# Kernel optimization log

Measured on AMD Instinct MI355X. Metric: run time of the kernel, lower is better.

The kernel has to match this reference:

```python
import jax, jax.numpy as jnp
import numpy as np


def setup_inputs() -> dict:
    key = jax.random.key(0)
    ks = jax.random.split(key, 8)
    B, N, D, S = 4, 16384, 512, 512
    x = jax.random.normal(ks[0], (B, N, D), dtype=jnp.float32)
    jx = jnp.sort(jax.random.randint(ks[1], (N,), 0, S, dtype=jnp.int64))
    scale = 1.0 / np.sqrt(D)
    Wf = jax.random.normal(ks[2], (D, D), dtype=jnp.float32) * scale
    bf = jax.random.normal(ks[3], (D,), dtype=jnp.float32) * scale
    Wg = jax.random.normal(ks[4], (D, D), dtype=jnp.float32) * scale
    bg = jax.random.normal(ks[5], (D,), dtype=jnp.float32) * scale
    Wh = jax.random.normal(ks[6], (D, D), dtype=jnp.float32) * scale
    bh = jax.random.normal(ks[7], (D,), dtype=jnp.float32) * scale
    return {"x": x, "jx": jx, "num_segments": S, "Wf": Wf, "bf": bf,
            "Wg": Wg, "bg": bg, "Wh": Wh, "bh": bh}


def reference(x, jx, num_segments, Wf, bf, Wg, bg, Wh, bh):
    # x: [B, N, D]; jx: [N] segment ids; segments along axis 1.
    fx = jnp.einsum('bnd,ed->bne', x, Wf) + bf  # f(x)
    gx = jnp.einsum('bnd,ed->bne', x, Wg) + bg  # g(x)
    # move N to leading axis so jax.ops.segment_* apply: [N, B, D]
    gx_t = jnp.transpose(gx, (1, 0, 2))
    fx_t = jnp.transpose(fx, (1, 0, 2))
    # scatter_softmax over segments (numerically stable)
    m = jax.ops.segment_max(gx_t, jx, num_segments=num_segments)  # [S, B, D]
    e = jnp.exp(gx_t - m[jx])
    denom = jax.ops.segment_sum(e, jx, num_segments=num_segments)  # [S, B, D]
    w = e / denom[jx]  # [N, B, D]
    # weighted scatter-sum
    y_t = jax.ops.segment_sum(fx_t * w, jx, num_segments=num_segments)  # [S, B, D]
    y = jnp.transpose(y_t, (1, 0, 2))  # [B, S, D]
    hy = jnp.einsum('bsd,ed->bse', y, Wh) + bh
    # expand=True: gather back to per-element
    return hy[:, jx]  # [B, N, D]
```

## Files before the change

kernel.cpp:

```cpp
#include <hip/hip_runtime.h>
#include <stdint.h>

#define B_ 4
#define N_ 16384
#define D_ 512
#define S_ 512

typedef __attribute__((ext_vector_type(8))) short bf16x8;
typedef __attribute__((ext_vector_type(4))) float f32x4;

__device__ __forceinline__ float bf2f(unsigned short u) {
  union { unsigned int i; float f; } v; v.i = ((unsigned int)u) << 16; return v.f;
}
__device__ __forceinline__ unsigned short f2bf(float f) {
  unsigned int x = __float_as_uint(f);
  return (unsigned short)((x + 0x7FFFu + ((x >> 16) & 1u)) >> 16);
}
__device__ __forceinline__ float ldf(const void* p, long i, bool f32) {
  return f32 ? ((const float*)p)[i] : bf2f(((const unsigned short*)p)[i]);
}
__device__ __forceinline__ void gl_lds16(void* lds_base, const void* g) {
  __builtin_amdgcn_global_load_lds(
      (const __attribute__((address_space(1))) unsigned int*)g,
      (__attribute__((address_space(3))) unsigned int*)lds_base,
      16, 0, 0);
}

__device__ __forceinline__ bool classify_f32(const unsigned short* x, int* cnt) {
  int c = 0;
#pragma unroll
  for (int i = 0; i < 8; i++) {
    unsigned short w = x[threadIdx.x * 8 + i];
    int e = (w >> 7) & 0xFF;
    if (e == 0 || (e >= 100 && e <= 140)) c++;
  }
  cnt[threadIdx.x] = c;
  __syncthreads();
  for (int s = 128; s > 0; s >>= 1) {
    if ((int)threadIdx.x < s) cnt[threadIdx.x] += cnt[threadIdx.x + s];
    __syncthreads();
  }
  bool f32 = cnt[0] < 1843;
  __syncthreads();
  return f32;
}

__device__ __forceinline__ bool jx_is_i64(const int* jx32) { return jx32[N_ - 1] == 0; }
__device__ __forceinline__ int seg_id(const int* jx32, int n, bool i64) {
  return i64 ? jx32[2 * n] : jx32[n];
}

__global__ __launch_bounds__(256)
void prep_all(const void* __restrict__ x, const int* __restrict__ jx,
              const void* __restrict__ Wf, const void* __restrict__ bfv,
              const void* __restrict__ Wg, const void* __restrict__ bgv,
              const void* __restrict__ Wh, const void* __restrict__ bhv,
              unsigned short* __restrict__ xb, unsigned short* __restrict__ Wfg,
              unsigned short* __restrict__ biasfg, unsigned short* __restrict__ Whb,
              unsigned short* __restrict__ bhb, int* __restrict__ segst) {
  const int blk = blockIdx.x, tid = threadIdx.x;
  if (blk >= 19462) {
    int s = (blk - 19462) * 256 + tid;
    if (s > S_) return;
    bool i64 = jx_is_i64(jx);
    int lo = 0, hi = N_;
    while (lo < hi) {
      int mid = (lo + hi) >> 1;
      if (seg_id(jx, mid, i64) < s) lo = mid + 1; else hi = mid;
    }
    segst[s] = lo;
    return;
  }
  __shared__ int cnt[256];
  const bool f32 = classify_f32((const unsigned short*)x, cnt);
  if (blk < 16384) {
    const size_t i0 = ((size_t)blk * 256 + tid) * 8;
    bf16x8 v;
    if (f32) {
      const float4* p = (const float4*)((const float*)x + i0);
      float4 a = p[0], b = p[1];
      v[0]=f2bf(a.x); v[1]=f2bf(a.y); v[2]=f2bf(a.z); v[3]=f2bf(a.w);
      v[4]=f2bf(b.x); v[5]=f2bf(b.y); v[6]=f2bf(b.z); v[7]=f2bf(b.w);
    } else {
      v = *(const bf16x8*)((const unsigned short*)x + i0);
    }
    *(bf16x8*)(xb + i0) = v;
  } else {
    int idx = (blk - 16384) * 256 + tid;
    if (idx < 524288) {
      int e = idx >> 9, d = idx & 511;
      float v = (e < 512) ? ldf(Wf, (long)e * 512 + d, f32)
                          : ldf(Wg, (long)(e - 512) * 512 + d, f32);
      Wfg[idx] = f2bf(v);
    } else if (idx < 786432) {
      Whb[idx - 524288] = f2bf(ldf(Wh, idx - 524288, f32));
    } else if (idx < 787456) {
      int j = idx - 786432;
      biasfg[j] = f2bf(j < 512 ? ldf(bfv, j, f32) : ldf(bgv, j - 512, f32));
    } else {
      bhb[idx - 787456] = f2bf(ldf(bhv, idx - 787456, f32));
    }
  }
}

#define BK 32

__global__ __launch_bounds__(256, 4)
void gemm_fg(const unsigned short* __restrict__ A, const unsigned short* __restrict__ Bm,
             const unsigned short* __restrict__ bias,
             unsigned short* __restrict__ Cf, unsigned short* __restrict__ Cg,
             int E, int Kdim, int splitcol, int tilesM, int tilesN) {
  __shared__ __align__(16) unsigned short As[128 * BK];
  __shared__ __align__(16) unsigned short Bs[128 * BK];
  const int L = blockIdx.x;
  const int xcd = L & 7, local = L >> 3;
  const int tm = xcd * (tilesM >> 3) + local / tilesN;
  const int tn = local % tilesN;
  const int m0 = tm * 128, n0 = tn * 128;

  const int tid  = threadIdx.x;
  const int w    = tid >> 6;
  const int lane = tid & 63;
  const int wm   = w >> 1, wn = w & 1;
  const int l15  = lane & 15, l4 = lane >> 4;
  const int srow = lane >> 2;
  const int scol = (lane & 3) * 8;

  f32x4 acc[4][4];
#pragma unroll
  for (int i = 0; i < 4; i++)
#pragma unroll
    for (int j = 0; j < 4; j++) acc[i][j] = (f32x4){0.f, 0.f, 0.f, 0.f};

  for (int kt = 0; kt < Kdim; kt += BK) {
    __syncthreads();
#pragma unroll
    for (int r = 0; r < 2; r++) {
      const int rb = (r * 4 + w) * 16;
      gl_lds16(&As[rb * BK], A + (size_t)(m0 + rb + srow) * Kdim + kt + scol);
      gl_lds16(&Bs[rb * BK], Bm + (size_t)(n0 + rb + srow) * Kdim + kt + scol);
    }
    __syncthreads();

    bf16x8 a[4], b[4];
#pragma unroll
    for (int i = 0; i < 4; i++)
      a[i] = *(const bf16x8*)&As[(wm * 64 + i * 16 + l15) * BK + l4 * 8];
#pragma unroll
    for (int j = 0; j < 4; j++)
      b[j] = *(const bf16x8*)&Bs[(wn * 64 + j * 16 + l15) * BK + l4 * 8];
#pragma unroll
    for (int i = 0; i < 4; i++)
#pragma unroll
      for (int j = 0; j < 4; j++)
        acc[i][j] = __builtin_amdgcn_mfma_f32_16x16x32_bf16(a[i], b[j], acc[i][j], 0, 0, 0);
  }

#pragma unroll
  for (int j = 0; j < 4; j++) {
    const int col = n0 + wn * 64 + j * 16 + l15;
    const float bv = bf2f(bias[col]);
    unsigned short* base; int cc, stride;
    if (col < splitcol) { base = Cf; cc = col; stride = splitcol; }
    else { base = Cg; cc = col - splitcol; stride = E - splitcol; }
#pragma unroll
    for (int i = 0; i < 4; i++) {
      const int rowb = m0 + wm * 64 + i * 16 + l4 * 4;
#pragma unroll
      for (int r = 0; r < 4; r++)
        base[(size_t)(rowb + r) * stride + cc] = f2bf(acc[i][j][r] + bv);
    }
  }
}

__global__ __launch_bounds__(256)
void seg_softmax(const unsigned short* __restrict__ f, const unsigned short* __restrict__ g,
                 const int* __restrict__ segst, unsigned short* __restrict__ y) {
  const int s = blockIdx.x * 2 + (threadIdx.x >> 7);
  const int b = blockIdx.y;
  const int d0 = (threadIdx.x & 127) * 4;
  const int st = segst[s], en = segst[s + 1];
  float den0=0.f, den1=0.f, den2=0.f, den3=0.f;
  float y0=0.f, y1=0.f, y2=0.f, y3=0.f;
  for (int n = st; n < en; n++) {
    const size_t off = (size_t)(b * N_ + n) * 512 + d0;
    const uint2 fp = *(const uint2*)(f + off);
    const uint2 gp = *(const uint2*)(g + off);
    const float f0 = bf2f((unsigned short)fp.x), f1 = bf2f((unsigned short)(fp.x >> 16));
    const float f2 = bf2f((unsigned short)fp.y), f3 = bf2f((unsigned short)(fp.y >> 16));
    const float g0 = bf2f((unsigned short)gp.x), g1 = bf2f((unsigned short)(gp.x >> 16));
    const float g2 = bf2f((unsigned short)gp.y), g3 = bf2f((unsigned short)(gp.y >> 16));
    const float e0 = __expf(g0), e1 = __expf(g1), e2 = __expf(g2), e3 = __expf(g3);
    den0 += e0; den1 += e1; den2 += e2; den3 += e3;
    y0 += f0 * e0; y1 += f1 * e1; y2 += f2 * e2; y3 += f3 * e3;
  }
  uint2 o;
  if (en > st) {
    o.x = (unsigned int)f2bf(y0 / den0) | ((unsigned int)f2bf(y1 / den1) << 16);
    o.y = (unsigned int)f2bf(y2 / den2) | ((unsigned int)f2bf(y3 / den3) << 16);
  } else { o.x = 0u; o.y = 0u; }
  *(uint2*)(y + (size_t)(b * S_ + s) * 512 + d0) = o;
}

__global__ __launch_bounds__(256)
void hy_gather(const unsigned short* __restrict__ y, const unsigned short* __restrict__ Whb,
               const unsigned short* __restrict__ bhb, const int* __restrict__ segst,
               const int* __restrict__ jx, const void* __restrict__ x,
               void* __restrict__ out) {
  __shared__ __align__(16) unsigned short As[64 * 32];
  __shared__ __align__(16) unsigned short Bs[64 * 32];
  __shared__ float hy_lds[64 * 64];
  __shared__ int cnt[256];
  const bool f32 = classify_f32((const unsigned short*)x, cnt);

  const int tid = threadIdx.x;
  const int w = tid >> 6, lane = tid & 63;
  const int l15 = lane & 15, l4 = lane >> 4;
  const int tr = blockIdx.x >> 3, tc = blockIdx.x & 7;
  const int m0 = tr * 64, c0 = tc * 64;
  const int b = m0 >> 9, s0 = m0 & 511;

  f32x4 acc[4];
#pragma unroll
  for (int j = 0; j < 4; j++) acc[j] = (f32x4){0.f, 0.f, 0.f, 0.f};

  const int srow = lane >> 2, scol = (lane & 3) * 8;
  for (int kt = 0; kt < 512; kt += 32) {
    __syncthreads();
    gl_lds16(&As[(w * 16) * 32], y   + (size_t)(m0 + w * 16 + srow) * 512 + kt + scol);
    gl_lds16(&Bs[(w * 16) * 32], Whb + (size_t)(c0 + w * 16 + srow) * 512 + kt + scol);
    __syncthreads();
    bf16x8 a = *(const bf16x8*)&As[(w * 16 + l15) * 32 + l4 * 8];
#pragma unroll
    for (int j = 0; j < 4; j++) {
      bf16x8 bb = *(const bf16x8*)&Bs[(j * 16 + l15) * 32 + l4 * 8];
      acc[j] = __builtin_amdgcn_mfma_f32_16x16x32_bf16(a, bb, acc[j], 0, 0, 0);
    }
  }
  __syncthreads();
#pragma unroll
  for (int j = 0; j < 4; j++) {
    const float bv = bf2f(bhb[c0 + j * 16 + l15]);
#pragma unroll
    for (int r = 0; r < 4; r++)
      hy_lds[(w * 16 + l4 * 4 + r) * 64 + j * 16 + l15] = acc[j][r] + bv;
  }
  __syncthreads();

  const int col = tid & 63, nstep = tid >> 6;
  for (int lr = 0; lr < 64; lr++) {
    const int st = segst[s0 + lr], en = segst[s0 + lr + 1];
    if (st >= en) continue;
    const float v = hy_lds[lr * 64 + col];
    if (f32) {
      float* o = (float*)out;
      for (int n = st + nstep; n < en; n += 4)
        o[((size_t)(b * N_ + n)) * 512 + c0 + col] = v;
    } else {
      unsigned short* o = (unsigned short*)out;
      const unsigned short vb = f2bf(v);
      for (int n = st + nstep; n < en; n += 4)
        o[((size_t)(b * N_ + n)) * 512 + c0 + col] = vb;
    }
  }
}

extern "C" void kernel_launch(void* const* d_in, const int* in_sizes, int n_in,
                              void* d_out, int out_size, void* d_ws, size_t ws_size,
                              hipStream_t stream) {
  const void* x  = d_in[0];
  const int* jx  = (const int*)d_in[1];
  const void* Wf = d_in[3];
  const void* bf = d_in[4];
  const void* Wg = d_in[5];
  const void* bg = d_in[6];
  const void* Wh = d_in[7];
  const void* bh = d_in[8];

  char* ws = (char*)d_ws;
  int* segst             = (int*)(ws + 4096);
  unsigned short* biasfg = (unsigned short*)(ws + 8192);
  unsigned short* bhb    = (unsigned short*)(ws + 16384);
  unsigned short* Wfg    = (unsigned short*)(ws + 32768);
  unsigned short* Whb    = (unsigned short*)(ws + 1081344);
  unsigned short* y_ws   = (unsigned short*)(ws + 1605632);
  unsigned short* xb     = (unsigned short*)(ws + 8388608);
  unsigned short* fbuf   = (unsigned short*)d_out;
  unsigned short* gbuf   = (unsigned short*)d_out + (size_t)B_ * N_ * D_;

  prep_all<<<19465, 256, 0, stream>>>(x, jx, Wf, bf, Wg, bg, Wh, bh,
                                      xb, Wfg, biasfg, Whb, bhb, segst);
  gemm_fg<<<4096, 256, 0, stream>>>(xb, Wfg, biasfg, fbuf, gbuf,
                                    1024, 512, 512, 512, 8);
  seg_softmax<<<dim3(256, B_), 256, 0, stream>>>(fbuf, gbuf, segst, y_ws);
  hy_gather<<<256, 256, 0, stream>>>(y_ws, Whb, bhb, segst, jx, x, d_out);
}
```

Baseline: 395.0 us.

## Fuse x fp32-to-bf16 conversion into GEMM A-load and split gather into separate kernel

Removes the separate pass that converted x to bf16 in workspace; the f/g GEMM now loads fp32 x directly and converts while staging into LDS. The dtype classification is computed once into a flag instead of in every block. The hy projection now writes to a workspace buffer, and a new fully parallel gather kernel writes the output with one wavefront per row and vectorized stores. This replaces the per-tile serial segment loop that used scalar stores. The trade-off is an extra launch plus a hy round-trip, and synchronous fp32 A loads in the GEMM in place of async global-to-LDS copies.

```diff
diff --git a/kernel.cpp b/kernel.cpp
--- a/kernel.cpp
+++ b/kernel.cpp
@@ -26,7 +26,15 @@
       16, 0, 0);
 }
 
-__device__ __forceinline__ bool classify_f32(const unsigned short* x, int* cnt) {
+__device__ __forceinline__ bool jx_is_i64(const int* jx32) { return jx32[N_ - 1] == 0; }
+__device__ __forceinline__ int seg_id(const int* jx32, int n, bool i64) {
+  return i64 ? jx32[2 * n] : jx32[n];
+}
+
+__global__ __launch_bounds__(256)
+void k0_flag_bounds(const unsigned short* __restrict__ x, const int* __restrict__ jx,
+                    int* __restrict__ flag, int* __restrict__ segst) {
+  __shared__ int cnt[256];
   int c = 0;
 #pragma unroll
   for (int i = 0; i < 8; i++) {
@@ -40,82 +48,56 @@
     if ((int)threadIdx.x < s) cnt[threadIdx.x] += cnt[threadIdx.x + s];
     __syncthreads();
   }
-  bool f32 = cnt[0] < 1843;
-  __syncthreads();
-  return f32;
-}
-
-__device__ __forceinline__ bool jx_is_i64(const int* jx32) { return jx32[N_ - 1] == 0; }
-__device__ __forceinline__ int seg_id(const int* jx32, int n, bool i64) {
-  return i64 ? jx32[2 * n] : jx32[n];
-}
-
-__global__ __launch_bounds__(256)
-void prep_all(const void* __restrict__ x, const int* __restrict__ jx,
-              const void* __restrict__ Wf, const void* __restrict__ bfv,
-              const void* __restrict__ Wg, const void* __restrict__ bgv,
-              const void* __restrict__ Wh, const void* __restrict__ bhv,
-              unsigned short* __restrict__ xb, unsigned short* __restrict__ Wfg,
-              unsigned short* __restrict__ biasfg, unsigned short* __restrict__ Whb,
-              unsigned short* __restrict__ bhb, int* __restrict__ segst) {
-  const int blk = blockIdx.x, tid = threadIdx.x;
-  if (blk >= 19462) {
-    int s = (blk - 19462) * 256 + tid;
-    if (s > S_) return;
-    bool i64 = jx_is_i64(jx);
-    int lo = 0, hi = N_;
-    while (lo < hi) {
-      int mid = (lo + hi) >> 1;
-      if (seg_id(jx, mid, i64) < s) lo = mid + 1; else hi = mid;
-    }
-    segst[s] = lo;
-    return;
-  }
-  __shared__ int cnt[256];
-  const bool f32 = classify_f32((const unsigned short*)x, cnt);
-  if (blk < 16384) {
-    const size_t i0 = ((size_t)blk * 256 + tid) * 8;
-    bf16x8 v;
-    if (f32) {
-      const float4* p = (const float4*)((const float*)x + i0);
-      float4 a = p[0], b = p[1];
-      v[0]=f2bf(a.x); v[1]=f2bf(a.y); v[2]=f2bf(a.z); v[3]=f2bf(a.w);
-      v[4]=f2bf(b.x); v[5]=f2bf(b.y); v[6]=f2bf(b.z); v[7]=f2bf(b.w);
-    } else {
-      v = *(const bf16x8*)((const unsigned short*)x + i0);
-    }
-    *(bf16x8*)(xb + i0) = v;
-  } else {
-    int idx = (blk - 16384) * 256 + tid;
-    if (idx < 524288) {
-      int e = idx >> 9, d = idx & 511;
-      float v = (e < 512) ? ldf(Wf, (long)e * 512 + d, f32)
-                          : ldf(Wg, (long)(e - 512) * 512 + d, f32);
-      Wfg[idx] = f2bf(v);
-    } else if (idx < 786432) {
-      Whb[idx - 524288] = f2bf(ldf(Wh, idx - 524288, f32));
-    } else if (idx < 787456) {
-      int j = idx - 786432;
-      biasfg[j] = f2bf(j < 512 ? ldf(bfv, j, f32) : ldf(bgv, j - 512, f32));
-    } else {
-      bhb[idx - 787456] = f2bf(ldf(bhv, idx - 787456, f32));
-    }
+  if (threadIdx.x == 0) flag[0] = (cnt[0] < 1843) ? 1 : 0;
+
+  const int s = blockIdx.x * 256 + threadIdx.x;
+  if (s > S_) return;
+  const bool i64 = jx_is_i64(jx);
+  int lo = 0, hi = N_;
+  while (lo < hi) {
+    int mid = (lo + hi) >> 1;
+    if (seg_id(jx, mid, i64) < s) lo = mid + 1; else hi = mid;
+  }
+  segst[s] = lo;
+}
+
+__global__ __launch_bounds__(256)
+void prep_w(const void* __restrict__ Wf, const void* __restrict__ bfv,
+            const void* __restrict__ Wg, const void* __restrict__ bgv,
+            const void* __restrict__ Wh, const void* __restrict__ bhv,
+            const int* __restrict__ flag,
+            unsigned short* __restrict__ Wfg, unsigned short* __restrict__ biasfg,
+            unsigned short* __restrict__ Whb, unsigned short* __restrict__ bhb) {
+  const bool f32 = flag[0] != 0;
+  int idx = blockIdx.x * 256 + threadIdx.x;
+  if (idx < 524288) {
+    int e = idx >> 9, d = idx & 511;
+    float v = (e < 512) ? ldf(Wf, (long)e * 512 + d, f32)
+                        : ldf(Wg, (long)(e - 512) * 512 + d, f32);
+    Wfg[idx] = f2bf(v);
+  } else if (idx < 786432) {
+    Whb[idx - 524288] = f2bf(ldf(Wh, idx - 524288, f32));
+  } else if (idx < 787456) {
+    int j = idx - 786432;
+    biasfg[j] = f2bf(j < 512 ? ldf(bfv, j, f32) : ldf(bgv, j - 512, f32));
+  } else if (idx < 787968) {
+    bhb[idx - 787456] = f2bf(ldf(bhv, idx - 787456, f32));
   }
 }
 
 #define BK 32
 
-__global__ __launch_bounds__(256, 4)
-void gemm_fg(const unsigned short* __restrict__ A, const unsigned short* __restrict__ Bm,
-             const unsigned short* __restrict__ bias,
-             unsigned short* __restrict__ Cf, unsigned short* __restrict__ Cg,
-             int E, int Kdim, int splitcol, int tilesM, int tilesN) {
+__global__ __launch_bounds__(256, 2)
+void gemm_fg(const void* __restrict__ A, const unsigned short* __restrict__ Bm,
+             const unsigned short* __restrict__ bias, const int* __restrict__ flag,
+             unsigned short* __restrict__ Cf, unsigned short* __restrict__ Cg) {
   __shared__ __align__(16) unsigned short As[128 * BK];
   __shared__ __align__(16) unsigned short Bs[128 * BK];
+  const bool af32 = flag[0] != 0;
   const int L = blockIdx.x;
   const int xcd = L & 7, local = L >> 3;
-  const int tm = xcd * (tilesM >> 3) + local / tilesN;
-  const int tn = local % tilesN;
+  const int tm = xcd * 64 + local / 8;
+  const int tn = local % 8;
   const int m0 = tm * 128, n0 = tn * 128;
 
   const int tid  = threadIdx.x;
@@ -125,6 +107,8 @@
   const int l15  = lane & 15, l4 = lane >> 4;
   const int srow = lane >> 2;
   const int scol = (lane & 3) * 8;
+  const int arow = tid >> 1;
+  const int ak0  = (tid & 1) * 16;
 
   f32x4 acc[4][4];
 #pragma unroll
@@ -132,43 +116,60 @@
 #pragma unroll
     for (int j = 0; j < 4; j++) acc[i][j] = (f32x4){0.f, 0.f, 0.f, 0.f};
 
-  for (int kt = 0; kt < Kdim; kt += BK) {
+  for (int kt = 0; kt < 512; kt += BK) {
     __syncthreads();
 #pragma unroll
     for (int r = 0; r < 2; r++) {
       const int rb = (r * 4 + w) * 16;
-      gl_lds16(&As[rb * BK], A + (size_t)(m0 + rb + srow) * Kdim + kt + scol);
-      gl_lds16(&Bs[rb * BK], Bm + (size_t)(n0 + rb + srow) * Kdim + kt + scol);
+      gl_lds16(&Bs[rb * BK], Bm + (size_t)(n0 + rb + srow) * 512 + kt + scol);
     }
-    __syncthreads();
-
-    bf16x8 a[4], b[4];
+    if (af32) {
+      const float4* ap = (const float4*)((const float*)A +
+                          (size_t)(m0 + arow) * 512 + kt + ak0);
+      float4 a0 = ap[0], a1 = ap[1], a2 = ap[2], a3 = ap[3];
+      bf16x8 v0, v1;
+      v0[0]=f2bf(a0.x); v0[1]=f2bf(a0.y); v0[2]=f2bf(a0.z); v0[3]=f2bf(a0.w);
+      v0[4]=f2bf(a1.x); v0[5]=f2bf(a1.y); v0[6]=f2bf(a1.z); v0[7]=f2bf(a1.w);
+      v1[0]=f2bf(a2.x); v1[1]=f2bf(a2.y); v1[2]=f2bf(a2.z); v1[3]=f2bf(a2.w);
+      v1[4]=f2bf(a3.x); v1[5]=f2bf(a3.y); v1[6]=f2bf(a3.z); v1[7]=f2bf(a3.w);
+      *(bf16x8*)&As[arow * BK + ak0]     = v0;
+      *(bf16x8*)&As[arow * BK + ak0 + 8] = v1;
+    } else {
+#pragma unroll
+      for (int r = 0; r < 2; r++) {
+        const int rb = (r * 4 + w) * 16;
+        gl_lds16(&As[rb * BK],
+                 (const unsigned short*)A + (size_t)(m0 + rb + srow) * 512 + kt + scol);
+      }
+    }
+    __syncthreads();
+
+    bf16x8 a[4], bb[4];
 #pragma unroll
     for (int i = 0; i < 4; i++)
       a[i] = *(const bf16x8*)&As[(wm * 64 + i * 16 + l15) * BK + l4 * 8];
 #pragma unroll
     for (int j = 0; j < 4; j++)
-      b[j] = *(const bf16x8*)&Bs[(wn * 64 + j * 16 + l15) * BK + l4 * 8];
+      bb[j] = *(const bf16x8*)&Bs[(wn * 64 + j * 16 + l15) * BK + l4 * 8];
 #pragma unroll
     for (int i = 0; i < 4; i++)
 #pragma unroll
       for (int j = 0; j < 4; j++)
-        acc[i][j] = __builtin_amdgcn_mfma_f32_16x16x32_bf16(a[i], b[j], acc[i][j], 0, 0, 0);
+        acc[i][j] = __builtin_amdgcn_mfma_f32_16x16x32_bf16(a[i], bb[j], acc[i][j], 0, 0, 0);
   }
 
 #pragma unroll
   for (int j = 0; j < 4; j++) {
     const int col = n0 + wn * 64 + j * 16 + l15;
     const float bv = bf2f(bias[col]);
-    unsigned short* base; int cc, stride;
-    if (col < splitcol) { base = Cf; cc = col; stride = splitcol; }
-    else { base = Cg; cc = col - splitcol; stride = E - splitcol; }
+    unsigned short* base = (col < 512) ? Cf : Cg;
+    const int cc = col & 511;
 #pragma unroll
     for (int i = 0; i < 4; i++) {
       const int rowb = m0 + wm * 64 + i * 16 + l4 * 4;
 #pragma unroll
       for (int r = 0; r < 4; r++)
-        base[(size_t)(rowb + r) * stride + cc] = f2bf(acc[i][j][r] + bv);
+        base[(size_t)(rowb + r) * 512 + cc] = f2bf(acc[i][j][r] + bv);
     }
   }
 }
@@ -203,28 +204,20 @@
 }
 
 __global__ __launch_bounds__(256)
-void hy_gather(const unsigned short* __restrict__ y, const unsigned short* __restrict__ Whb,
-               const unsigned short* __restrict__ bhb, const int* __restrict__ segst,
-               const int* __restrict__ jx, const void* __restrict__ x,
-               void* __restrict__ out) {
+void gemm_hy(const unsigned short* __restrict__ y, const unsigned short* __restrict__ Whb,
+             const unsigned short* __restrict__ bhb, unsigned short* __restrict__ hy) {
   __shared__ __align__(16) unsigned short As[64 * 32];
   __shared__ __align__(16) unsigned short Bs[64 * 32];
-  __shared__ float hy_lds[64 * 64];
-  __shared__ int cnt[256];
-  const bool f32 = classify_f32((const unsigned short*)x, cnt);
-
   const int tid = threadIdx.x;
   const int w = tid >> 6, lane = tid & 63;
   const int l15 = lane & 15, l4 = lane >> 4;
-  const int tr = blockIdx.x >> 3, tc = blockIdx.x & 7;
-  const int m0 = tr * 64, c0 = tc * 64;
-  const int b = m0 >> 9, s0 = m0 & 511;
+  const int m0 = (blockIdx.x >> 3) * 64, c0 = (blockIdx.x & 7) * 64;
+  const int srow = lane >> 2, scol = (lane & 3) * 8;
 
   f32x4 acc[4];
 #pragma unroll
   for (int j = 0; j < 4; j++) acc[j] = (f32x4){0.f, 0.f, 0.f, 0.f};
 
-  const int srow = lane >> 2, scol = (lane & 3) * 8;
   for (int kt = 0; kt < 512; kt += 32) {
     __syncthreads();
     gl_lds16(&As[(w * 16) * 32], y   + (size_t)(m0 + w * 16 + srow) * 512 + kt + scol);
@@ -237,31 +230,39 @@
       acc[j] = __builtin_amdgcn_mfma_f32_16x16x32_bf16(a, bb, acc[j], 0, 0, 0);
     }
   }
-  __syncthreads();
 #pragma unroll
   for (int j = 0; j < 4; j++) {
     const float bv = bf2f(bhb[c0 + j * 16 + l15]);
 #pragma unroll
     for (int r = 0; r < 4; r++)
-      hy_lds[(w * 16 + l4 * 4 + r) * 64 + j * 16 + l15] = acc[j][r] + bv;
-  }
-  __syncthreads();
-
-  const int col = tid & 63, nstep = tid >> 6;
-  for (int lr = 0; lr < 64; lr++) {
-    const int st = segst[s0 + lr], en = segst[s0 + lr + 1];
-    if (st >= en) continue;
-    const float v = hy_lds[lr * 64 + col];
-    if (f32) {
-      float* o = (float*)out;
-      for (int n = st + nstep; n < en; n += 4)
-        o[((size_t)(b * N_ + n)) * 512 + c0 + col] = v;
-    } else {
-      unsigned short* o = (unsigned short*)out;
-      const unsigned short vb = f2bf(v);
-      for (int n = st + nstep; n < en; n += 4)
-        o[((size_t)(b * N_ + n)) * 512 + c0 + col] = vb;
-    }
+      hy[(size_t)(m0 + w * 16 + l4 * 4 + r) * 512 + c0 + j * 16 + l15] =
+          f2bf(acc[j][r] + bv);
+  }
+}
+
+__global__ __launch_bounds__(256)
+void gather_out(const unsigned short* __restrict__ hy, const int* __restrict__ jx,
+                void* __restrict__ out, const int* __restrict__ flag) {
+  const bool f32 = flag[0] != 0;
+  const int gid  = blockIdx.x * 256 + threadIdx.x;
+  const int wid  = gid >> 6;
+  const int lane = gid & 63;
+  const int b = wid >> 14;
+  const int n = wid & (N_ - 1);
+  const bool i64 = jx_is_i64(jx);
+  const int s = seg_id(jx, n, i64);
+  const bf16x8 v = *(const bf16x8*)(hy + (size_t)(b * S_ + s) * 512 + lane * 8);
+  if (f32) {
+    float* dst = (float*)out + (size_t)wid * 512 + lane * 8;
+    float4 lo, hi;
+    lo.x=bf2f((unsigned short)v[0]); lo.y=bf2f((unsigned short)v[1]);
+    lo.z=bf2f((unsigned short)v[2]); lo.w=bf2f((unsigned short)v[3]);
+    hi.x=bf2f((unsigned short)v[4]); hi.y=bf2f((unsigned short)v[5]);
+    hi.z=bf2f((unsigned short)v[6]); hi.w=bf2f((unsigned short)v[7]);
+    *(float4*)dst = lo;
+    *(float4*)(dst + 4) = hi;
+  } else {
+    *(bf16x8*)((unsigned short*)out + (size_t)wid * 512 + lane * 8) = v;
   }
 }
 
@@ -278,20 +279,22 @@
   const void* bh = d_in[8];
 
   char* ws = (char*)d_ws;
+  int* flag              = (int*)(ws + 0);
   int* segst             = (int*)(ws + 4096);
   unsigned short* biasfg = (unsigned short*)(ws + 8192);
   unsigned short* bhb    = (unsigned short*)(ws + 16384);
   unsigned short* Wfg    = (unsigned short*)(ws + 32768);
   unsigned short* Whb    = (unsigned short*)(ws + 1081344);
   unsigned short* y_ws   = (unsigned short*)(ws + 1605632);
-  unsigned short* xb     = (unsigned short*)(ws + 8388608);
+  unsigned short* hy_ws  = (unsigned short*)(ws + 3702784);
   unsigned short* fbuf   = (unsigned short*)d_out;
   unsigned short* gbuf   = (unsigned short*)d_out + (size_t)B_ * N_ * D_;
 
-  prep_all<<<19465, 256, 0, stream>>>(x, jx, Wf, bf, Wg, bg, Wh, bh,
-                                      xb, Wfg, biasfg, Whb, bhb, segst);
-  gemm_fg<<<4096, 256, 0, stream>>>(xb, Wfg, biasfg, fbuf, gbuf,
-                                    1024, 512, 512, 512, 8);
+  k0_flag_bounds<<<3, 256, 0, stream>>>((const unsigned short*)x, jx, flag, segst);
+  prep_w<<<3078, 256, 0, stream>>>(Wf, bf, Wg, bg, Wh, bh, flag,
+                                   Wfg, biasfg, Whb, bhb);
+  gemm_fg<<<4096, 256, 0, stream>>>(x, Wfg, biasfg, flag, fbuf, gbuf);
   seg_softmax<<<dim3(256, B_), 256, 0, stream>>>(fbuf, gbuf, segst, y_ws);
-  hy_gather<<<256, 256, 0, stream>>>(y_ws, Whb, bhb, segst, jx, x, d_out);
-}
+  gemm_hy<<<256, 256, 0, stream>>>(y_ws, Whb, bhb, hy_ws);
+  gather_out<<<16384, 256, 0, stream>>>(hy_ws, jx, d_out, flag);
+}
```

Result: slower. 417.1 us (+5.6%).
